# Kernel optimization log

Hardware: AMD Instinct MI355X
Metric: run time of the kernel (lower is better)

Reference implementation:

```python
import jax, jax.numpy as jnp
import numpy as np

B, S, HID = 4, 1024, 1024
NH, HD = 16, 64  # num heads, head dim


def setup_inputs() -> dict:
    key = jax.random.key(0)
    ks = jax.random.split(key, 8)
    scale = 0.02
    return {
        "hidden_states": jax.random.normal(ks[0], (B, S, HID), dtype=jnp.float32),
        "attention_mask": jnp.ones((B, 1, 1, S), dtype=jnp.float32),
        "Wq": jax.random.normal(ks[1], (HID, HID), dtype=jnp.float32) * scale,
        "bq": jnp.zeros((HID,), dtype=jnp.float32),
        "Wk": jax.random.normal(ks[2], (HID, HID), dtype=jnp.float32) * scale,
        "bk": jnp.zeros((HID,), dtype=jnp.float32),
        "Wv": jax.random.normal(ks[3], (HID, HID), dtype=jnp.float32) * scale,
        "bv": jnp.zeros((HID,), dtype=jnp.float32),
    }


def reference(hidden_states, attention_mask, Wq, bq, Wk, bk, Wv, bv):
    # Linear projections: torch nn.Linear computes x @ W.T + b
    q = hidden_states @ Wq.T + bq  # [B,S,HID]
    k = hidden_states @ Wk.T + bk
    v = hidden_states @ Wv.T + bv

    def split_heads(x):
        return x.reshape(B, S, NH, HD).transpose(0, 2, 1, 3)  # [B,NH,S,HD]

    q, k, v = split_heads(q), split_heads(k), split_heads(v)

    scores = jnp.einsum("bhqd,bhkd->bhqk", q, k) / jnp.sqrt(jnp.float32(HD))
    # faithful to original: scores - (2 - mask) * 1e6
    scores = scores - (2.0 - attention_mask) * 1.0e6
    probs = jax.nn.softmax(scores, axis=-1)
    # dropout: eval mode -> identity
    ctx = jnp.einsum("bhqk,bhkd->bhqd", probs, v)  # [B,NH,S,HD]
    ctx = ctx.transpose(0, 2, 1, 3).reshape(B, S, HID)
    return ctx
```

## Files before the change

kernel.cpp:

```cpp
#include <hip/hip_runtime.h>
#include <math.h>

#define B_ 4
#define S_ 1024
#define HID_ 1024
#define NH_ 16
#define HD_ 64
#define NTOK (B_ * S_)

typedef __attribute__((ext_vector_type(4))) float f32x4;
typedef __attribute__((ext_vector_type(16))) float f32x16;
typedef __attribute__((ext_vector_type(8))) short bf16x8;

__device__ __forceinline__ unsigned short f2bf(float f) {
    union { float f; unsigned int u; } v; v.f = f;
    unsigned int r = v.u + 0x7fffu + ((v.u >> 16) & 1u);
    return (unsigned short)(r >> 16);
}

#if __has_builtin(__builtin_amdgcn_cvt_pk_bf16_f32)
__device__ __forceinline__ unsigned int pk_bf16(float a, float b) {
    auto v = __builtin_amdgcn_cvt_pk_bf16_f32(a, b);
    union { decltype(v) v; unsigned int u; } cv; cv.v = v;
    return cv.u;
}
#else
__device__ __forceinline__ unsigned int pk_bf16(float a, float b) {
    return (unsigned int)f2bf(a) | ((unsigned int)f2bf(b) << 16);
}
#endif

#if __has_builtin(__builtin_amdgcn_permlane32_swap)
__device__ __forceinline__ void plswap(unsigned &a, unsigned &b) {
    typedef __attribute__((ext_vector_type(2))) int v2i;
    v2i r = __builtin_amdgcn_permlane32_swap((int)a, (int)b, false, false);
    a = (unsigned)r[0]; b = (unsigned)r[1];
}
#else
__device__ __forceinline__ void plswap(unsigned &a, unsigned &b) {
    const unsigned bl = __shfl_xor(b, 32);
    const unsigned ah = __shfl_xor(a, 32);
    const bool hi = ((threadIdx.x & 63) >> 5) != 0;
    const unsigned na = hi ? bl : a;
    const unsigned nb = hi ? b  : ah;
    a = na; b = nb;
}
#endif

__device__ __forceinline__ void load_lds16(const void* g, void* l) {
    __builtin_amdgcn_global_load_lds(
        (const __attribute__((address_space(1))) unsigned int*)(uintptr_t)g,
        (__attribute__((address_space(3))) unsigned int*)(uintptr_t)l,
        16, 0, 0);
}

__global__ __launch_bounds__(256) void cvt_all(
    const float* __restrict__ x, const float* __restrict__ wq,
    const float* __restrict__ wk, const float* __restrict__ wv,
    unsigned short* __restrict__ xb, unsigned short* __restrict__ wqb,
    unsigned short* __restrict__ wkb, unsigned short* __restrict__ wvb)
{
    const int which = blockIdx.y;
    const float* src = which == 0 ? x : which == 1 ? wq : which == 2 ? wk : wv;
    unsigned short* dst = which == 0 ? xb : which == 1 ? wqb : which == 2 ? wkb : wvb;
    const int n4 = (which == 0) ? (NTOK * HID_ / 4) : (HID_ * HID_ / 4);
    int i = blockIdx.x * 256 + threadIdx.x;
    if (i < n4) {
        float4 f = ((const float4*)src)[i];
        uint2 o;
        o.x = pk_bf16(f.x, f.y);
        o.y = pk_bf16(f.z, f.w);
        ((uint2*)dst)[i] = o;
    }
}

__global__ __launch_bounds__(512, 6) void qkv_gemm_mfma(
    const unsigned short* __restrict__ xb,
    const unsigned short* __restrict__ Wqb, const float* __restrict__ bq,
    const unsigned short* __restrict__ Wkb, const float* __restrict__ bk,
    const unsigned short* __restrict__ Wvb, const float* __restrict__ bv,
    unsigned short* __restrict__ qout, unsigned short* __restrict__ kout,
    unsigned short* __restrict__ vtout)
{
    const int which = blockIdx.z;
    const unsigned short* __restrict__ W = which == 0 ? Wqb : which == 1 ? Wkb : Wvb;
    const float* __restrict__ bias       = which == 0 ? bq  : which == 1 ? bk  : bv;

    __shared__ unsigned short As[128 * 64];
    __shared__ unsigned short Bs[128 * 64];

    const int t    = threadIdx.x;
    const int lane = t & 63;
    const int w    = t >> 6;
    const int wr   = w >> 2;
    const int wc   = w & 3;
    const int g    = lane >> 4;
    const int lrow = lane & 15;

    const int bm = blockIdx.x;
    const int bn = blockIdx.y;

    const unsigned short* __restrict__ Arow = (which == 2) ? W  : xb;
    const unsigned short* __restrict__ Brow = (which == 2) ? xb : W;
    const int am0 = (which == 2) ? bn * 128 : bm * 128;
    const int bn0 = (which == 2) ? bm * 128 : bn * 128;

    const int srow = t >> 3;
    const int sc   = ((t & 7) ^ ((t >> 3) & 7)) << 3;
    const unsigned short* gA = Arow + (size_t)(am0 + srow) * HID_ + sc;
    const unsigned short* gB = Brow + (size_t)(bn0 + srow) * HID_ + sc;

    const f32x4 zero = {0.f, 0.f, 0.f, 0.f};
    f32x4 acc[4][2];
    #pragma unroll
    for (int i = 0; i < 4; ++i)
        #pragma unroll
        for (int j = 0; j < 2; ++j) acc[i][j] = zero;

    for (int k0 = 0; k0 < HID_; k0 += 64) {
        __syncthreads();
        #pragma unroll
        for (int i = 0; i < 2; ++i) {
            load_lds16(gA + (size_t)(i * 64) * HID_ + k0, (char*)As + i * 8192 + t * 16);
            load_lds16(gB + (size_t)(i * 64) * HID_ + k0, (char*)Bs + i * 8192 + t * 16);
        }
        __syncthreads();

        #pragma unroll
        for (int ks = 0; ks < 2; ++ks) {
            bf16x8 af[4], bf[2];
            #pragma unroll
            for (int i = 0; i < 4; ++i) {
                const int row = wr * 64 + i * 16 + lrow;
                af[i] = *(const bf16x8*)&As[row * 64 + (((ks * 4 + g) ^ (row & 7)) << 3)];
            }
            #pragma unroll
            for (int j = 0; j < 2; ++j) {
                const int row = wc * 32 + j * 16 + lrow;
                bf[j] = *(const bf16x8*)&Bs[row * 64 + (((ks * 4 + g) ^ (row & 7)) << 3)];
            }
            #pragma unroll
            for (int i = 0; i < 4; ++i)
                #pragma unroll
                for (int j = 0; j < 2; ++j)
                    acc[i][j] = __builtin_amdgcn_mfma_f32_16x16x32_bf16(
                        af[i], bf[j], acc[i][j], 0, 0, 0);
        }
    }

    const int col   = lane & 15;
    const int rbase = (lane >> 4) << 2;
    if (which == 2) {
        #pragma unroll
        for (int i = 0; i < 4; ++i) {
            #pragma unroll
            for (int r = 0; r < 4; ++r) {
                const int feat = bn * 128 + wr * 64 + i * 16 + rbase + r;
                const int h = feat >> 6, d = feat & 63;
                const float bias_v = bias[feat];
                #pragma unroll
                for (int j = 0; j < 2; ++j) {
                    const int tok = bm * 128 + wc * 32 + j * 16 + col;
                    const int b = tok >> 10, s = tok & 1023;
                    vtout[((size_t)((b << 4) + h) << 16) + ((size_t)d << 10) + s] =
                        f2bf(acc[i][j][r] + bias_v);
                }
            }
        }
    } else {
        #pragma unroll
        for (int j = 0; j < 2; ++j) {
            const int feat = bn * 128 + wc * 32 + j * 16 + col;
            const int h = feat >> 6, d = feat & 63;
            const float bias_v = bias[feat];
            #pragma unroll
            for (int i = 0; i < 4; ++i) {
                const int tok0 = bm * 128 + wr * 64 + i * 16 + rbase;
                #pragma unroll
                for (int r = 0; r < 4; ++r) {
                    const int tok = tok0 + r;
                    const int b = tok >> 10, s = tok & 1023;
                    const size_t off = ((size_t)((b << 4) + h) << 16) + ((size_t)s << 6) + d;
                    const float val = acc[i][j][r] + bias_v;
                    if (which == 0) qout[off] = f2bf(val);
                    else            kout[off] = f2bf(val);
                }
            }
        }
    }
}

__global__ __launch_bounds__(512, 4) void attn_mfma(
    const unsigned short* __restrict__ Q, const unsigned short* __restrict__ K,
    const unsigned short* __restrict__ Vt, const float* __restrict__ mask,
    float* __restrict__ out)
{
    __shared__ unsigned short Ks[2][2][64 * 64];
    __shared__ unsigned short Vts[2][64 * 64];
    __shared__ float Mts[1024];

    const int t    = threadIdx.x;
    const int lane = t & 63;
    const int w    = t >> 6;
    const int kh   = w >> 2;
    const int pw   = w & 3;
    const int q31  = lane & 31;
    const int hl   = lane >> 5;

    const int bh = blockIdx.x;
    const int b  = bh >> 4;
    const int h  = bh & 15;
    const int q0w = (blockIdx.y << 7) + (pw << 5);

    const unsigned short* __restrict__ qg = Q  + ((size_t)bh << 16);
    const unsigned short* __restrict__ kg = K  + ((size_t)bh << 16);
    const unsigned short* __restrict__ vg = Vt + ((size_t)bh << 16);

    bf16x8 qreg[4];
    {
        const unsigned short* qp = qg + ((size_t)(q0w + q31) << 6);
        #pragma unroll
        for (int kc = 0; kc < 4; ++kc)
            qreg[kc] = *(const bf16x8*)&qp[kc * 16 + (hl << 3)];
    }

    int fro[4];
    #pragma unroll
    for (int kc = 0; kc < 4; ++kc)
        fro[kc] = q31 * 128 + ((((kc << 1) + hl) ^ (q31 & 7)) << 4);

    const int srow = t >> 3;
    const int c8   = ((t & 7) ^ (srow & 7)) << 3;
    const unsigned short* kstat = kg + (size_t)srow * 64 + c8;
    const unsigned short* vstat = vg + (size_t)srow * 1024 + c8;

    f32x16 O[2];
    #pragma unroll
    for (int i = 0; i < 16; ++i) { O[0][i] = 0.f; O[1][i] = 0.f; }
    float lacc = 0.f;

    #pragma unroll
    for (int hh = 0; hh < 2; ++hh)
        load_lds16(kstat + hh * 32768, (char*)Ks[hh][0] + t * 16);
    #pragma unroll
    for (int i = 0; i < 2; ++i) {
        const int key = t + i * 512;
        Mts[key] = (2.0f - mask[(b << 10) + key]) * 1.0e6f;
    }
    __syncthreads();

    for (int kt = 0; kt < 8; ++kt) {
        const int cur = kt & 1;

        #pragma unroll
        for (int hh = 0; hh < 2; ++hh) {
            load_lds16(vstat + hh * 512 + (size_t)kt * 64, (char*)Vts[hh] + t * 16);
            if (kt < 7)
                load_lds16(kstat + hh * 32768 + (size_t)(kt + 1) * 4096,
                           (char*)Ks[hh][cur ^ 1] + t * 16);
        }

        const char* Kb = (const char*)Ks[kh][cur];
        const char* Vb = (const char*)Vts[kh];

        f32x16 sacc[2];
        #pragma unroll
        for (int i = 0; i < 16; ++i) { sacc[0][i] = 0.f; sacc[1][i] = 0.f; }
        #pragma unroll
        for (int kb = 0; kb < 2; ++kb) {
            bf16x8 kf[4];
            #pragma unroll
            for (int kc = 0; kc < 4; ++kc)
                kf[kc] = *(const bf16x8*)(Kb + kb * 4096 + fro[kc]);
            __builtin_amdgcn_s_setprio(1);
            #pragma unroll
            for (int kc = 0; kc < 4; ++kc)
                sacc[kb] = __builtin_amdgcn_mfma_f32_32x32x16_bf16(
                    kf[kc], qreg[kc], sacc[kb], 0, 0, 0);
            __builtin_amdgcn_s_setprio(0);
        }

        bf16x8 pf[4];
        #pragma unroll
        for (int kb = 0; kb < 2; ++kb) {
            unsigned u[4][2];
            #pragma unroll
            for (int rq = 0; rq < 4; ++rq) {
                const f32x4 m4 = *(const f32x4*)&Mts[(kh << 9) + kt * 64 + kb * 32 + rq * 8 + (hl << 2)];
                float p[4];
                #pragma unroll
                for (int r = 0; r < 4; ++r) {
                    const float sv = sacc[kb][rq * 4 + r] * 0.125f - m4[r];
                    p[r] = __expf(sv + 1.0e6f);
                }
                lacc += (p[0] + p[1]) + (p[2] + p[3]);
                u[rq][0] = pk_bf16(p[0], p[1]);
                u[rq][1] = pk_bf16(p[2], p[3]);
            }
            #pragma unroll
            for (int c = 0; c < 2; ++c) {
                unsigned w0 = u[2 * c][0], w2 = u[2 * c + 1][0];
                plswap(w0, w2);
                unsigned w1 = u[2 * c][1], w3 = u[2 * c + 1][1];
                plswap(w1, w3);
                union { unsigned uu[4]; bf16x8 v; } f;
                f.uu[0] = w0; f.uu[1] = w1; f.uu[2] = w2; f.uu[3] = w3;
                pf[kb * 2 + c] = f.v;
            }
        }

        __syncthreads();

        #pragma unroll
        for (int hb = 0; hb < 2; ++hb) {
            bf16x8 vf[4];
            #pragma unroll
            for (int kc = 0; kc < 4; ++kc)
                vf[kc] = *(const bf16x8*)(Vb + hb * 4096 + fro[kc]);
            __builtin_amdgcn_s_setprio(1);
            #pragma unroll
            for (int kc = 0; kc < 4; ++kc)
                O[hb] = __builtin_amdgcn_mfma_f32_32x32x16_bf16(
                    pf[kc], vf[kc], O[hb], 0, 0, 0);
            __builtin_amdgcn_s_setprio(0);
        }

        __syncthreads();
    }

    float* Osh = (float*)&Ks[0][0][0];
    float* Lsh = (float*)&Vts[0][0];
    const float l = lacc + __shfl_xor(lacc, 32);
    if (kh == 1) {
        #pragma unroll
        for (int r = 0; r < 16; ++r) {
            const int qr = (r & 3) + ((r >> 2) << 3) + (hl << 2);
            Osh[pw * 2048 + qr * 64 + q31]      = O[0][r];
            Osh[pw * 2048 + qr * 64 + 32 + q31] = O[1][r];
        }
        if (lane < 32) Lsh[pw * 32 + q31] = l;
    } else {
        if (lane < 32) Lsh[128 + pw * 32 + q31] = l;
    }
    __syncthreads();
    if (kh == 0) {
        #pragma unroll
        for (int r = 0; r < 16; ++r) {
            const int qr = (r & 3) + ((r >> 2) << 3) + (hl << 2);
            const float inv = 1.0f / (Lsh[128 + pw * 32 + qr] + Lsh[pw * 32 + qr]);
            const size_t base = (((size_t)(b << 10) + (q0w + qr)) << 10) + (h << 6);
            out[base + q31]      = (O[0][r] + Osh[pw * 2048 + qr * 64 + q31])      * inv;
            out[base + 32 + q31] = (O[1][r] + Osh[pw * 2048 + qr * 64 + 32 + q31]) * inv;
        }
    }
}

extern "C" void kernel_launch(void* const* d_in, const int* in_sizes, int n_in,
                              void* d_out, int out_size, void* d_ws, size_t ws_size,
                              hipStream_t stream) {
    const float* hs   = (const float*)d_in[0];
    const float* mask = (const float*)d_in[1];
    const float* Wq   = (const float*)d_in[2];
    const float* bq   = (const float*)d_in[3];
    const float* Wk   = (const float*)d_in[4];
    const float* bk   = (const float*)d_in[5];
    const float* Wv   = (const float*)d_in[6];
    const float* bv   = (const float*)d_in[7];
    float* out = (float*)d_out;

    char* ws = (char*)d_ws;
    unsigned short* xb  = (unsigned short*)(ws);
    unsigned short* wqb = (unsigned short*)(ws + ((size_t)8  << 20));
    unsigned short* wkb = (unsigned short*)(ws + ((size_t)10 << 20));
    unsigned short* wvb = (unsigned short*)(ws + ((size_t)12 << 20));
    unsigned short* qb  = (unsigned short*)(ws + ((size_t)14 << 20));
    unsigned short* kb  = (unsigned short*)(ws + ((size_t)22 << 20));
    unsigned short* vtb = (unsigned short*)(ws + ((size_t)30 << 20));

    cvt_all<<<dim3(4096, 4), 256, 0, stream>>>(hs, Wq, Wk, Wv, xb, wqb, wkb, wvb);
    qkv_gemm_mfma<<<dim3(NTOK / 128, HID_ / 128, 3), 512, 0, stream>>>(
        xb, wqb, bq, wkb, bk, wvb, bv, qb, kb, vtb);
    attn_mfma<<<dim3(B_ * NH_, S_ / 128), 512, 0, stream>>>(qb, kb, vtb, mask, out);
}
```

Measured before the change: 147.7 us.

## Rewrite QKV GEMM with 256x256 tiles and double-buffered LDS prefetch pipeline

```diff
diff --git a/kernel.cpp b/kernel.cpp
--- a/kernel.cpp
+++ b/kernel.cpp
@@ -74,7 +74,7 @@
     }
 }
 
-__global__ __launch_bounds__(512, 6) void qkv_gemm_mfma(
+__global__ __launch_bounds__(512, 2) void qkv_gemm_mfma(
     const unsigned short* __restrict__ xb,
     const unsigned short* __restrict__ Wqb, const float* __restrict__ bq,
     const unsigned short* __restrict__ Wkb, const float* __restrict__ bk,
@@ -82,12 +82,11 @@
     unsigned short* __restrict__ qout, unsigned short* __restrict__ kout,
     unsigned short* __restrict__ vtout)
 {
+    extern __shared__ char sm[];
+
     const int which = blockIdx.z;
     const unsigned short* __restrict__ W = which == 0 ? Wqb : which == 1 ? Wkb : Wvb;
     const float* __restrict__ bias       = which == 0 ? bq  : which == 1 ? bk  : bv;
-
-    __shared__ unsigned short As[128 * 64];
-    __shared__ unsigned short Bs[128 * 64];
 
     const int t    = threadIdx.x;
     const int lane = t & 63;
@@ -97,54 +96,124 @@
     const int g    = lane >> 4;
     const int lrow = lane & 15;
 
-    const int bm = blockIdx.x;
-    const int bn = blockIdx.y;
-
     const unsigned short* __restrict__ Arow = (which == 2) ? W  : xb;
     const unsigned short* __restrict__ Brow = (which == 2) ? xb : W;
-    const int am0 = (which == 2) ? bn * 128 : bm * 128;
-    const int bn0 = (which == 2) ? bm * 128 : bn * 128;
-
-    const int srow = t >> 3;
-    const int sc   = ((t & 7) ^ ((t >> 3) & 7)) << 3;
-    const unsigned short* gA = Arow + (size_t)(am0 + srow) * HID_ + sc;
-    const unsigned short* gB = Brow + (size_t)(bn0 + srow) * HID_ + sc;
-
-    const f32x4 zero = {0.f, 0.f, 0.f, 0.f};
-    f32x4 acc[4][2];
+    const int am0 = (which == 2) ? blockIdx.y * 256 : blockIdx.x * 256;
+    const int bn0 = (which == 2) ? blockIdx.x * 256 : blockIdx.y * 256;
+
+    const int r0  = t >> 2;
+    const int c0  = t & 3;
+    const int csw = (c0 ^ (r0 & 3)) << 3;
+    const unsigned short* gA = Arow + (size_t)(am0 + r0) * HID_ + csw;
+    const unsigned short* gB = Brow + (size_t)(bn0 + r0) * HID_ + csw;
+
+    const int sw4  = (g ^ (lane & 3)) << 4;
+    const int aoff = wr * 8192 + lrow * 64 + sw4;
+    const int boff = wc * 4096 + lrow * 64 + sw4;
+
+    f32x4 acc[8][4];
     #pragma unroll
-    for (int i = 0; i < 4; ++i)
-        #pragma unroll
-        for (int j = 0; j < 2; ++j) acc[i][j] = zero;
-
-    for (int k0 = 0; k0 < HID_; k0 += 64) {
-        __syncthreads();
-        #pragma unroll
-        for (int i = 0; i < 2; ++i) {
-            load_lds16(gA + (size_t)(i * 64) * HID_ + k0, (char*)As + i * 8192 + t * 16);
-            load_lds16(gB + (size_t)(i * 64) * HID_ + k0, (char*)Bs + i * 8192 + t * 16);
-        }
-        __syncthreads();
-
-        #pragma unroll
-        for (int ks = 0; ks < 2; ++ks) {
-            bf16x8 af[4], bf[2];
-            #pragma unroll
-            for (int i = 0; i < 4; ++i) {
-                const int row = wr * 64 + i * 16 + lrow;
-                af[i] = *(const bf16x8*)&As[row * 64 + (((ks * 4 + g) ^ (row & 7)) << 3)];
-            }
-            #pragma unroll
-            for (int j = 0; j < 2; ++j) {
-                const int row = wc * 32 + j * 16 + lrow;
-                bf[j] = *(const bf16x8*)&Bs[row * 64 + (((ks * 4 + g) ^ (row & 7)) << 3)];
-            }
-            #pragma unroll
-            for (int i = 0; i < 4; ++i)
-                #pragma unroll
-                for (int j = 0; j < 2; ++j)
-                    acc[i][j] = __builtin_amdgcn_mfma_f32_16x16x32_bf16(
-                        af[i], bf[j], acc[i][j], 0, 0, 0);
+    for (int m = 0; m < 8; ++m)
+        #pragma unroll
+        for (int n = 0; n < 4; ++n) acc[m][n] = (f32x4){0.f, 0.f, 0.f, 0.f};
+
+    auto stageA = [&](int nb, int ks, int kt1) {
+        char* dst = sm + ((nb * 2 + ks) << 14);
+        const unsigned short* s = gA + kt1 * 64 + ks * 32;
+        load_lds16(s, dst + t * 16);
+        load_lds16(s + (size_t)128 * HID_, dst + (t + 512) * 16);
+    };
+    auto stageB = [&](int nb, int ks, int kt1) {
+        char* dst = sm + 65536 + ((nb * 2 + ks) << 14);
+        const unsigned short* s = gB + kt1 * 64 + ks * 32;
+        load_lds16(s, dst + t * 16);
+        load_lds16(s + (size_t)128 * HID_, dst + (t + 512) * 16);
+    };
+
+    stageA(0, 0, 0); stageB(0, 0, 0); stageA(0, 1, 0); stageB(0, 1, 0);
+    asm volatile("s_waitcnt vmcnt(4)" ::: "memory");
+    __builtin_amdgcn_s_barrier();
+
+    for (int kt = 0; kt < 16; ++kt) {
+        const int cur = kt & 1, nb = cur ^ 1;
+        const bool nl = (kt < 15);
+        const char* A0 = sm + ((cur * 2 + 0) << 14);
+        const char* A1 = sm + ((cur * 2 + 1) << 14);
+        const char* B0 = sm + 65536 + ((cur * 2 + 0) << 14);
+        const char* B1 = sm + 65536 + ((cur * 2 + 1) << 14);
+        bf16x8 bf[4];
+
+        {
+            bf16x8 af[4];
+            #pragma unroll
+            for (int m = 0; m < 4; ++m) af[m] = *(const bf16x8*)(A0 + aoff + m * 1024);
+            #pragma unroll
+            for (int n = 0; n < 4; ++n) bf[n] = *(const bf16x8*)(B0 + boff + n * 1024);
+            if (nl) stageA(nb, 0, kt + 1);
+            __builtin_amdgcn_s_barrier();
+            __builtin_amdgcn_s_setprio(1);
+            #pragma unroll
+            for (int m = 0; m < 4; ++m)
+                #pragma unroll
+                for (int n = 0; n < 4; ++n)
+                    acc[m][n] = __builtin_amdgcn_mfma_f32_16x16x32_bf16(
+                        af[m], bf[n], acc[m][n], 0, 0, 0);
+            __builtin_amdgcn_s_setprio(0);
+        }
+        {
+            bf16x8 af[4];
+            #pragma unroll
+            for (int m = 0; m < 4; ++m) af[m] = *(const bf16x8*)(A0 + aoff + (4 + m) * 1024);
+            if (nl) {
+                stageB(nb, 0, kt + 1);
+                asm volatile("s_waitcnt vmcnt(4)" ::: "memory");
+            } else {
+                asm volatile("s_waitcnt vmcnt(0)" ::: "memory");
+            }
+            __builtin_amdgcn_s_barrier();
+            __builtin_amdgcn_s_setprio(1);
+            #pragma unroll
+            for (int m = 0; m < 4; ++m)
+                #pragma unroll
+                for (int n = 0; n < 4; ++n)
+                    acc[4 + m][n] = __builtin_amdgcn_mfma_f32_16x16x32_bf16(
+                        af[m], bf[n], acc[4 + m][n], 0, 0, 0);
+            __builtin_amdgcn_s_setprio(0);
+        }
+        {
+            bf16x8 af[4];
+            #pragma unroll
+            for (int m = 0; m < 4; ++m) af[m] = *(const bf16x8*)(A1 + aoff + m * 1024);
+            #pragma unroll
+            for (int n = 0; n < 4; ++n) bf[n] = *(const bf16x8*)(B1 + boff + n * 1024);
+            if (nl) stageA(nb, 1, kt + 1);
+            __builtin_amdgcn_s_barrier();
+            __builtin_amdgcn_s_setprio(1);
+            #pragma unroll
+            for (int m = 0; m < 4; ++m)
+                #pragma unroll
+                for (int n = 0; n < 4; ++n)
+                    acc[m][n] = __builtin_amdgcn_mfma_f32_16x16x32_bf16(
+                        af[m], bf[n], acc[m][n], 0, 0, 0);
+            __builtin_amdgcn_s_setprio(0);
+        }
+        {
+            bf16x8 af[4];
+            #pragma unroll
+            for (int m = 0; m < 4; ++m) af[m] = *(const bf16x8*)(A1 + aoff + (4 + m) * 1024);
+            if (nl) {
+                stageB(nb, 1, kt + 1);
+                asm volatile("s_waitcnt vmcnt(4)" ::: "memory");
+            }
+            __builtin_amdgcn_s_barrier();
+            __builtin_amdgcn_s_setprio(1);
+            #pragma unroll
+            for (int m = 0; m < 4; ++m)
+                #pragma unroll
+                for (int n = 0; n < 4; ++n)
+                    acc[4 + m][n] = __builtin_amdgcn_mfma_f32_16x16x32_bf16(
+                        af[m], bf[n], acc[4 + m][n], 0, 0, 0);
+            __builtin_amdgcn_s_setprio(0);
         }
     }
 
@@ -152,36 +221,35 @@
     const int rbase = (lane >> 4) << 2;
     if (which == 2) {
         #pragma unroll
-        for (int i = 0; i < 4; ++i) {
-            #pragma unroll
-            for (int r = 0; r < 4; ++r) {
-                const int feat = bn * 128 + wr * 64 + i * 16 + rbase + r;
+        for (int m = 0; m < 8; ++m) {
+            #pragma unroll
+            for (int rr = 0; rr < 4; ++rr) {
+                const int feat = am0 + wr * 128 + m * 16 + rbase + rr;
                 const int h = feat >> 6, d = feat & 63;
                 const float bias_v = bias[feat];
                 #pragma unroll
-                for (int j = 0; j < 2; ++j) {
-                    const int tok = bm * 128 + wc * 32 + j * 16 + col;
+                for (int n = 0; n < 4; ++n) {
+                    const int tok = bn0 + wc * 64 + n * 16 + col;
                     const int b = tok >> 10, s = tok & 1023;
                     vtout[((size_t)((b << 4) + h) << 16) + ((size_t)d << 10) + s] =
-                        f2bf(acc[i][j][r] + bias_v);
+                        f2bf(acc[m][n][rr] + bias_v);
                 }
             }
         }
     } else {
         #pragma unroll
-        for (int j = 0; j < 2; ++j) {
-            const int feat = bn * 128 + wc * 32 + j * 16 + col;
+        for (int n = 0; n < 4; ++n) {
+            const int feat = bn0 + wc * 64 + n * 16 + col;
             const int h = feat >> 6, d = feat & 63;
             const float bias_v = bias[feat];
             #pragma unroll
-            for (int i = 0; i < 4; ++i) {
-                const int tok0 = bm * 128 + wr * 64 + i * 16 + rbase;
-                #pragma unroll
-                for (int r = 0; r < 4; ++r) {
-                    const int tok = tok0 + r;
+            for (int m = 0; m < 8; ++m) {
+                #pragma unroll
+                for (int rr = 0; rr < 4; ++rr) {
+                    const int tok = am0 + wr * 128 + m * 16 + rbase + rr;
                     const int b = tok >> 10, s = tok & 1023;
                     const size_t off = ((size_t)((b << 4) + h) << 16) + ((size_t)s << 6) + d;
-                    const float val = acc[i][j][r] + bias_v;
+                    const float val = acc[m][n][rr] + bias_v;
                     if (which == 0) qout[off] = f2bf(val);
                     else            kout[off] = f2bf(val);
                 }
@@ -377,8 +445,15 @@
     unsigned short* kb  = (unsigned short*)(ws + ((size_t)22 << 20));
     unsigned short* vtb = (unsigned short*)(ws + ((size_t)30 << 20));
 
+    static bool attr_set = false;
+    if (!attr_set) {
+        hipFuncSetAttribute((const void*)qkv_gemm_mfma,
+                            hipFuncAttributeMaxDynamicSharedMemorySize, 131072);
+        attr_set = true;
+    }
+
     cvt_all<<<dim3(4096, 4), 256, 0, stream>>>(hs, Wq, Wk, Wv, xb, wqb, wkb, wvb);
-    qkv_gemm_mfma<<<dim3(NTOK / 128, HID_ / 128, 3), 512, 0, stream>>>(
+    qkv_gemm_mfma<<<dim3(NTOK / 256, HID_ / 256, 3), 512, 131072, stream>>>(
         xb, wqb, bq, wkb, bk, wvb, bv, qb, kb, vtb);
     attn_mfma<<<dim3(B_ * NH_, S_ / 128), 512, 0, stream>>>(qb, kb, vtb, mask, out);
 }
```

After: 148.1 us. About the same (+0.3%).
